# Performance work log

Measured on AMD Instinct MI355X. Metric: run time of the kernel, lower is better.

Reference implementation:

```python
import jax, jax.numpy as jnp
import numpy as np

B, C, H, W = 16, 32, 32, 2048


def setup_inputs() -> dict:
    key = jax.random.key(0)
    ks = jax.random.split(key, 7)
    s = 1.0 / np.sqrt(C * H)  # torch conv2d default init scale (fan_in = C*H*1)
    x = jax.random.normal(ks[0], (B, C, H, W), dtype=jnp.float32)
    wq = jax.random.uniform(ks[1], (C, C, H), jnp.float32, -s, s)
    bq = jax.random.uniform(ks[2], (C,), jnp.float32, -s, s)
    wk = jax.random.uniform(ks[3], (C, C, H), jnp.float32, -s, s)
    bk = jax.random.uniform(ks[4], (C,), jnp.float32, -s, s)
    wv = jax.random.uniform(ks[5], (C, C, H), jnp.float32, -s, s)
    bv = jax.random.uniform(ks[6], (C,), jnp.float32, -s, s)
    return {"x": x, "wq": wq, "bq": bq, "wk": wk, "bk": bk, "wv": wv, "bv": bv}


def _proj(x, w, b):
    # Conv2d kernel (H,1) with no padding == contract over (in_channels, H).
    # x: [B,C,H,W], w: [Cout,Cin,H] -> [B,Cout,W]
    return jnp.einsum('bihw,oih->bow', x, w) + b[None, :, None]


def reference(x, wq, bq, wk, bk, wv, bv):
    q = _proj(x, wq, bq)            # [B,C,W]
    k = _proj(x, wk, bk)            # [B,C,W]
    v = _proj(x, wv, bv)            # [B,C,W]
    # query.permute(0,2,1) @ key -> [B,W,W]; NOTE: unscaled, as in source.
    scores = jnp.einsum('bcw,bcv->bwv', q, k)
    attn = jax.nn.softmax(scores, axis=-1)
    # value @ attention^T -> [B,C,W]
    out = jnp.einsum('bcv,bwv->bcw', v, attn)
    # bilinear upsample (1,W)->(H,W), align_corners=False: width is identity,
    # height replicates the single row -> pure broadcast. Then residual add.
    return out[:, :, None, :] + x
```

## Files before the change

kernel.cpp:

```cpp
#include <hip/hip_runtime.h>
#include <hip/hip_bf16.h>

typedef __bf16 bf16x8 __attribute__((ext_vector_type(8)));
typedef float  f32x4  __attribute__((ext_vector_type(4)));
typedef float  f32x16 __attribute__((ext_vector_type(16)));

#define NB 16
#define NC 32
#define NH 32
#define NW 2048
#define NK (NC*NH)
#define LOG2E 1.4426950408889634f

static __device__ __forceinline__ unsigned int pk2(float a, float b) {
    union { __bf16 h[2]; unsigned int u; } z;
    z.h[0] = (__bf16)a; z.h[1] = (__bf16)b;
    return z.u;
}

__global__ __launch_bounds__(256) void wprep_kernel(
    const float* __restrict__ wq, const float* __restrict__ wk,
    const float* __restrict__ wv, __bf16* __restrict__ wb)
{
    const int i = blockIdx.x * 256 + threadIdx.x;
    const float* srcs[3] = { wq, wk, wv };
    float4 v = *(const float4*)(srcs[i >> 13] + (size_t)(i & 8191) * 4);
    const float sc = (i >> 13) == 0 ? LOG2E : 1.0f;
    union { __bf16 h[4]; unsigned long long u; } z;
    z.h[0] = (__bf16)(v.x * sc); z.h[1] = (__bf16)(v.y * sc);
    z.h[2] = (__bf16)(v.z * sc); z.h[3] = (__bf16)(v.w * sc);
    *(unsigned long long*)(wb + (size_t)i * 4) = z.u;
}

__global__ __launch_bounds__(256) void proj_kernel(
    const float* __restrict__ x, const __bf16* __restrict__ wb,
    const float* __restrict__ bq, const float* __restrict__ bk,
    const float* __restrict__ bv,
    __bf16* __restrict__ qT, __bf16* __restrict__ kT, __bf16* __restrict__ V)
{
    const int b    = blockIdx.x >> 6;
    const int wt   = blockIdx.x & 63;
    const int wave = threadIdx.x >> 6;
    const int lane = threadIdx.x & 63;
    const int g    = lane >> 4;
    const int lr   = lane & 15;
    const int w0   = wt * 32;

    __shared__ __align__(16) char smem_raw[24576];
    __bf16 (*stage)[2][32][40] = reinterpret_cast<__bf16(*)[2][32][40]>(smem_raw);
    f32x4 (*part)[6][64] = reinterpret_cast<f32x4(*)[6][64]>(smem_raw);

    const float* xb = x + (size_t)b * NK * NW;
    const int k0 = wave * 256;

    const int skr = lane >> 3;
    const int swq = lane & 7;
    const float* xs = xb + w0 + swq * 4;

    f32x4 acc[2][6];
    #pragma unroll
    for (int mt = 0; mt < 2; ++mt)
        #pragma unroll
        for (int nt = 0; nt < 6; ++nt)
            acc[mt][nt] = f32x4{0.f, 0.f, 0.f, 0.f};

    float4 xv[4];

#define LOADX(STEP)                                                           \
    _Pragma("unroll")                                                         \
    for (int r4 = 0; r4 < 4; ++r4)                                            \
        xv[r4] = *(const float4*)(xs + (size_t)(k0 + (STEP)*32 + r4*8 + skr) * NW);

#define WRITEX(BUF)                                                           \
    _Pragma("unroll")                                                         \
    for (int r4 = 0; r4 < 4; ++r4) {                                          \
        const int kl = r4*8 + skr;                                            \
        __bf16* wp = &stage[wave][BUF][swq*4][kl];                            \
        wp[0]   = (__bf16)xv[r4].x;                                           \
        wp[40]  = (__bf16)xv[r4].y;                                           \
        wp[80]  = (__bf16)xv[r4].z;                                           \
        wp[120] = (__bf16)xv[r4].w;                                           \
    }

#define COMPUTE(BUF, KK)                                                      \
    {                                                                         \
        const bf16x8 af0 = *(const bf16x8*)&stage[wave][BUF][lr][g*8];        \
        const bf16x8 af1 = *(const bf16x8*)&stage[wave][BUF][16 + lr][g*8];   \
        bf16x8 bfv[6];                                                        \
        _Pragma("unroll")                                                     \
        for (int nt = 0; nt < 6; ++nt)                                        \
            bfv[nt] = *(const bf16x8*)(wb + (size_t)(nt >> 1) * 32768         \
                                          + (size_t)((nt & 1) * 16 + lr) * NK \
                                          + (KK) + g*8);                      \
        _Pragma("unroll")                                                     \
        for (int nt = 0; nt < 6; ++nt) {                                      \
            acc[0][nt] = __builtin_amdgcn_mfma_f32_16x16x32_bf16(             \
                af0, bfv[nt], acc[0][nt], 0, 0, 0);                           \
            acc[1][nt] = __builtin_amdgcn_mfma_f32_16x16x32_bf16(             \
                af1, bfv[nt], acc[1][nt], 0, 0, 0);                           \
        }                                                                     \
    }

    LOADX(0); WRITEX(0);
    LOADX(1);
    #pragma unroll
    for (int s = 0; s < 8; ++s) {
        const int cb = s & 1;
        if (s < 7) { WRITEX(cb ^ 1); }
        if (s < 6) { LOADX(s + 2); }
        COMPUTE(cb, k0 + s*32);
    }
#undef LOADX
#undef WRITEX
#undef COMPUTE

    const float* biases[3] = { bq, bk, bv };
    #pragma unroll
    for (int mt = 0; mt < 2; ++mt) {
        __syncthreads();
        #pragma unroll
        for (int nt = 0; nt < 6; ++nt)
            part[wave][nt][lane] = acc[mt][nt];
        __syncthreads();
        #pragma unroll
        for (int q = 0; q < 2; ++q) {
            const int nt = wave + q * 4;
            if (nt < 6) {
                f32x4 s = part[0][nt][lane];
                #pragma unroll
                for (int sl = 1; sl < 4; ++sl) s += part[sl][nt][lane];
                const int pid = nt >> 1;
                const int o   = (nt & 1) * 16 + lr;
                float bb = biases[pid][o];
                if (pid == 0) bb *= LOG2E;
                if (pid < 2) {
                    __bf16* dst = (pid ? kT : qT) + (size_t)b * NW * NC;
                    #pragma unroll
                    for (int r = 0; r < 4; ++r) {
                        const int w = w0 + mt*16 + g*4 + r;
                        dst[(size_t)w * NC + o] = (__bf16)(s[r] + bb);
                    }
                } else {
                    union { __bf16 h[4]; unsigned long long u; } z;
                    #pragma unroll
                    for (int r = 0; r < 4; ++r) z.h[r] = (__bf16)(s[r] + bb);
                    __bf16* dst = V + ((size_t)b * NC + o) * NW + (w0 + mt*16 + g*4);
                    *(unsigned long long*)dst = z.u;
                }
            }
        }
    }
}

__global__ __launch_bounds__(256) void attn_kernel(
    const float* __restrict__ x,
    const __bf16* __restrict__ qT, const __bf16* __restrict__ kT,
    const __bf16* __restrict__ V,
    float* __restrict__ out)
{
    const int b    = blockIdx.x >> 6;
    const int wt   = blockIdx.x & 63;
    const int w0   = wt * 32;
    const int wave = threadIdx.x >> 6;
    const int lane = threadIdx.x & 63;
    const int wl = lane & 31, hi = lane >> 5;
    const int swl = (wl & 0x13) | ((wl & 4) << 1) | ((wl & 8) >> 1);

    const __bf16* qTb = qT + (size_t)b * NW * NC;
    const __bf16* kTb = kT + (size_t)b * NW * NC;
    const __bf16* Vb  = V  + (size_t)b * NC * NW;

    const __bf16* qrow = qTb + (size_t)(w0 + wl) * NC;
    const bf16x8 qf0 = *(const bf16x8*)(qrow + hi*8);
    const bf16x8 qf1 = *(const bf16x8*)(qrow + 16 + hi*8);

    f32x16 acc, z16;
    #pragma unroll
    for (int r = 0; r < 16; ++r) { acc[r] = 0.f; z16[r] = 0.f; }
    float lsum = 0.f;

    const int vbeg = wave * 512;
    const __bf16* kbase = kTb + (size_t)swl * NC;
    const __bf16* vbase = Vb + (size_t)wl * NW;

#define KLD0(V0) (*(const bf16x8*)(kbase + (size_t)(V0) * NC + hi*8))
#define KLD1(V0) (*(const bf16x8*)(kbase + (size_t)(V0) * NC + 16 + hi*8))
#define VLD0(V0) (*(const bf16x8*)(vbase + (V0) + hi*8))
#define VLD1(V0) (*(const bf16x8*)(vbase + (V0) + 16 + hi*8))

    bf16x8 k0r = KLD0(vbeg), k1r = KLD1(vbeg);
    f32x16 s_cur = __builtin_amdgcn_mfma_f32_32x32x16_bf16(k0r, qf0, z16, 0, 0, 0);
    s_cur = __builtin_amdgcn_mfma_f32_32x32x16_bf16(k1r, qf1, s_cur, 0, 0, 0);
    k0r = KLD0(vbeg + 32); k1r = KLD1(vbeg + 32);
    bf16x8 v0r = VLD0(vbeg), v1r = VLD1(vbeg);

    #pragma unroll
    for (int it = 0; it < 16; ++it) {
        f32x16 s_next;
        if (it < 15) {
            s_next = __builtin_amdgcn_mfma_f32_32x32x16_bf16(k0r, qf0, z16, 0, 0, 0);
            s_next = __builtin_amdgcn_mfma_f32_32x32x16_bf16(k1r, qf1, s_next, 0, 0, 0);
        }
        if (it < 14) {
            const int vn = vbeg + (it + 2) * 32;
            k0r = KLD0(vn); k1r = KLD1(vn);
        }

        float p[16];
        #pragma unroll
        for (int r = 0; r < 16; ++r) p[r] = __builtin_amdgcn_exp2f(s_cur[r]);
        float ts[8];
        #pragma unroll
        for (int r = 0; r < 8; ++r) ts[r] = p[r] + p[r+8];
        #pragma unroll
        for (int r = 0; r < 4; ++r) ts[r] += ts[r+4];
        lsum += (ts[0] + ts[1]) + (ts[2] + ts[3]);

        union { unsigned int u[4]; bf16x8 v; } pfa, pfb;
        #pragma unroll
        for (int i = 0; i < 4; ++i) pfa.u[i] = pk2(p[2*i],     p[2*i + 1]);
        #pragma unroll
        for (int i = 0; i < 4; ++i) pfb.u[i] = pk2(p[8 + 2*i], p[8 + 2*i + 1]);

        acc = __builtin_amdgcn_mfma_f32_32x32x16_bf16(v0r, pfa.v, acc, 0, 0, 0);
        acc = __builtin_amdgcn_mfma_f32_32x32x16_bf16(v1r, pfb.v, acc, 0, 0, 0);

        if (it < 15) {
            const int vn = vbeg + (it + 1) * 32;
            v0r = VLD0(vn); v1r = VLD1(vn);
            s_cur = s_next;
        }
    }
#undef KLD0
#undef KLD1
#undef VLD0
#undef VLD1
    lsum += __shfl_xor(lsum, 32);

    __shared__ float sl[4][32];
    __shared__ float sO[4][32][33];
    __shared__ float Of[32][33];

    if (hi == 0) sl[wave][wl] = lsum;
    #pragma unroll
    for (int r = 0; r < 16; ++r) {
        const int c = (r & 3) + 8*(r >> 2) + 4*hi;
        sO[wave][c][wl] = acc[r];
    }
    __syncthreads();

    {
        const int w  = threadIdx.x & 31;
        const int cg = threadIdx.x >> 5;
        const float L = (sl[0][w] + sl[1][w]) + (sl[2][w] + sl[3][w]);
        const float rL = 1.0f / L;
        #pragma unroll
        for (int cc = 0; cc < 4; ++cc) {
            const int c = cg * 4 + cc;
            const float o = ((sO[0][c][w] + sO[1][c][w]) +
                             (sO[2][c][w] + sO[3][c][w]));
            Of[c][w] = o * rL;
        }
    }
    __syncthreads();

    const float* xb = x   + (size_t)b * NC * NH * NW + w0;
    float*       ob = out + (size_t)b * NC * NH * NW + w0;
    const int chunk = threadIdx.x & 7;
    #pragma unroll
    for (int it = 0; it < 32; ++it) {
        const int row = it*32 + (threadIdx.x >> 3);
        const int c = row >> 5, h = row & 31;
        const size_t off = ((size_t)c * NH + h) * NW + chunk*4;
        const f32x4 xv = *(const f32x4*)(xb + off);
        f32x4 ov;
        ov[0] = Of[c][chunk*4 + 0] + xv[0];
        ov[1] = Of[c][chunk*4 + 1] + xv[1];
        ov[2] = Of[c][chunk*4 + 2] + xv[2];
        ov[3] = Of[c][chunk*4 + 3] + xv[3];
        __builtin_nontemporal_store(ov, (f32x4*)(ob + off));
    }
}

extern "C" void kernel_launch(void* const* d_in, const int* in_sizes, int n_in,
                              void* d_out, int out_size, void* d_ws, size_t ws_size,
                              hipStream_t stream)
{
    const float* x  = (const float*)d_in[0];
    const float* wq = (const float*)d_in[1];
    const float* bq = (const float*)d_in[2];
    const float* wk = (const float*)d_in[3];
    const float* bk = (const float*)d_in[4];
    const float* wv = (const float*)d_in[5];
    const float* bv = (const float*)d_in[6];
    float* out = (float*)d_out;

    char* ws = (char*)d_ws;
    __bf16* qT = (__bf16*)(ws);
    __bf16* kT = (__bf16*)(ws + (2u << 20));
    __bf16* V  = (__bf16*)(ws + (4u << 20));
    __bf16* wb = (__bf16*)(ws + (6u << 20));

    hipLaunchKernelGGL(wprep_kernel, dim3(96), dim3(256), 0, stream, wq, wk, wv, wb);
    hipLaunchKernelGGL(proj_kernel, dim3(NB * 64), dim3(256), 0, stream,
                       x, wb, bq, bk, bv, qT, kT, V);
    hipLaunchKernelGGL(attn_kernel, dim3(NB * 64), dim3(256), 0, stream,
                       x, qT, kT, V, out);
}
```

Baseline: 99.12 us.

## Stage full x tile in LDS cooperatively before projection MFMA loop

The projection kernel stops using per-wave double-buffered register/LDS staging of x. Instead the whole block first loads the 32-column by 1024-K x tile into a padded bf16 LDS tile, synchronizes once, then runs the MFMA loop reading straight from LDS. This removes the software pipeline and its bookkeeping and gives more memory-level parallelism in the load phase. In exchange, loads no longer overlap compute, and LDS use grows to about 65 KB, which can lower occupancy.

```diff
diff --git a/kernel.cpp b/kernel.cpp
--- a/kernel.cpp
+++ b/kernel.cpp
@@ -11,6 +11,7 @@
 #define NW 2048
 #define NK (NC*NH)
 #define LOG2E 1.4426950408889634f
+#define TPAD 1040
 
 static __device__ __forceinline__ unsigned int pk2(float a, float b) {
     union { __bf16 h[2]; unsigned int u; } z;
@@ -46,17 +47,31 @@
     const int lr   = lane & 15;
     const int w0   = wt * 32;
 
-    __shared__ __align__(16) char smem_raw[24576];
-    __bf16 (*stage)[2][32][40] = reinterpret_cast<__bf16(*)[2][32][40]>(smem_raw);
+    __shared__ __align__(16) char smem_raw[32 * TPAD * 2];
+    __bf16 (*tile)[TPAD] = reinterpret_cast<__bf16(*)[TPAD]>(smem_raw);
     f32x4 (*part)[6][64] = reinterpret_cast<f32x4(*)[6][64]>(smem_raw);
 
     const float* xb = x + (size_t)b * NK * NW;
+
+    {
+        const int swq = threadIdx.x & 7;
+        const int skr = threadIdx.x >> 3;
+        const float* xs = xb + w0 + swq * 4;
+        __bf16* wp0 = &tile[swq * 4][skr];
+        #pragma unroll 8
+        for (int pass = 0; pass < 32; ++pass) {
+            const int k = pass * 32 + skr;
+            const float4 v = *(const float4*)(xs + (size_t)k * NW);
+            __bf16* wp = wp0 + pass * 32;
+            wp[0*TPAD] = (__bf16)v.x;
+            wp[1*TPAD] = (__bf16)v.y;
+            wp[2*TPAD] = (__bf16)v.z;
+            wp[3*TPAD] = (__bf16)v.w;
+        }
+    }
+    __syncthreads();
+
     const int k0 = wave * 256;
-
-    const int skr = lane >> 3;
-    const int swq = lane & 7;
-    const float* xs = xb + w0 + swq * 4;
-
     f32x4 acc[2][6];
     #pragma unroll
     for (int mt = 0; mt < 2; ++mt)
@@ -64,55 +79,25 @@
         for (int nt = 0; nt < 6; ++nt)
             acc[mt][nt] = f32x4{0.f, 0.f, 0.f, 0.f};
 
-    float4 xv[4];
-
-#define LOADX(STEP)                                                           \
-    _Pragma("unroll")                                                         \
-    for (int r4 = 0; r4 < 4; ++r4)                                            \
-        xv[r4] = *(const float4*)(xs + (size_t)(k0 + (STEP)*32 + r4*8 + skr) * NW);
-
-#define WRITEX(BUF)                                                           \
-    _Pragma("unroll")                                                         \
-    for (int r4 = 0; r4 < 4; ++r4) {                                          \
-        const int kl = r4*8 + skr;                                            \
-        __bf16* wp = &stage[wave][BUF][swq*4][kl];                            \
-        wp[0]   = (__bf16)xv[r4].x;                                           \
-        wp[40]  = (__bf16)xv[r4].y;                                           \
-        wp[80]  = (__bf16)xv[r4].z;                                           \
-        wp[120] = (__bf16)xv[r4].w;                                           \
-    }
-
-#define COMPUTE(BUF, KK)                                                      \
-    {                                                                         \
-        const bf16x8 af0 = *(const bf16x8*)&stage[wave][BUF][lr][g*8];        \
-        const bf16x8 af1 = *(const bf16x8*)&stage[wave][BUF][16 + lr][g*8];   \
-        bf16x8 bfv[6];                                                        \
-        _Pragma("unroll")                                                     \
-        for (int nt = 0; nt < 6; ++nt)                                        \
-            bfv[nt] = *(const bf16x8*)(wb + (size_t)(nt >> 1) * 32768         \
-                                          + (size_t)((nt & 1) * 16 + lr) * NK \
-                                          + (KK) + g*8);                      \
-        _Pragma("unroll")                                                     \
-        for (int nt = 0; nt < 6; ++nt) {                                      \
-            acc[0][nt] = __builtin_amdgcn_mfma_f32_16x16x32_bf16(             \
-                af0, bfv[nt], acc[0][nt], 0, 0, 0);                           \
-            acc[1][nt] = __builtin_amdgcn_mfma_f32_16x16x32_bf16(             \
-                af1, bfv[nt], acc[1][nt], 0, 0, 0);                           \
-        }                                                                     \
-    }
-
-    LOADX(0); WRITEX(0);
-    LOADX(1);
     #pragma unroll
     for (int s = 0; s < 8; ++s) {
-        const int cb = s & 1;
-        if (s < 7) { WRITEX(cb ^ 1); }
-        if (s < 6) { LOADX(s + 2); }
-        COMPUTE(cb, k0 + s*32);
-    }
-#undef LOADX
-#undef WRITEX
-#undef COMPUTE
+        const int kk = k0 + s * 32;
+        const bf16x8 af0 = *(const bf16x8*)&tile[lr][kk + g*8];
+        const bf16x8 af1 = *(const bf16x8*)&tile[16 + lr][kk + g*8];
+        bf16x8 bfv[6];
+        #pragma unroll
+        for (int nt = 0; nt < 6; ++nt)
+            bfv[nt] = *(const bf16x8*)(wb + (size_t)(nt >> 1) * 32768
+                                          + (size_t)((nt & 1) * 16 + lr) * NK
+                                          + kk + g*8);
+        #pragma unroll
+        for (int nt = 0; nt < 6; ++nt) {
+            acc[0][nt] = __builtin_amdgcn_mfma_f32_16x16x32_bf16(
+                af0, bfv[nt], acc[0][nt], 0, 0, 0);
+            acc[1][nt] = __builtin_amdgcn_mfma_f32_16x16x32_bf16(
+                af1, bfv[nt], acc[1][nt], 0, 0, 0);
+        }
+    }
 
     const float* biases[3] = { bq, bk, bv };
     #pragma unroll
```

Measured after the change: 109.1 us. 1.1x slower.
